# Kernel tuning notes

Hardware: AMD Instinct MI355X
Metric: run time of the kernel (lower is better)

Reference implementation:

```python
import jax, jax.numpy as jnp
import numpy as np

B, S, D, H = 2, 2048, 1024, 16

def setup_inputs() -> dict:
    key = jax.random.key(0)
    ks = jax.random.split(key, 5)
    s = 0.02
    return {
        "x": jax.random.normal(ks[0], (B, S, D), dtype=jnp.float32),
        "Wq": jax.random.normal(ks[1], (D, D), dtype=jnp.float32) * s,
        "bq": jnp.zeros((D,), dtype=jnp.float32),
        "Wk": jax.random.normal(ks[2], (D, D), dtype=jnp.float32) * s,
        "bk": jnp.zeros((D,), dtype=jnp.float32),
        "Wv": jax.random.normal(ks[3], (D, D), dtype=jnp.float32) * s,
        "bv": jnp.zeros((D,), dtype=jnp.float32),
        "Wp": jax.random.normal(ks[4], (D, D), dtype=jnp.float32) * s,
        "bp": jnp.zeros((D,), dtype=jnp.float32),
    }

def reference(x, Wq, bq, Wk, bk, Wv, bv, Wp, bp):
    b, s, d = x.shape
    hd = d // H
    # QKV projections, split into heads: [b, H, s, hd]
    q = (x @ Wq.T + bq).reshape(b, s, H, hd).transpose(0, 2, 1, 3)
    k = (x @ Wk.T + bk).reshape(b, s, H, hd).transpose(0, 2, 1, 3)
    v = (x @ Wv.T + bv).reshape(b, s, H, hd).transpose(0, 2, 1, 3)
    # NOTE: original scales by 1/sqrt(embedding_size), not head_dim
    att = jnp.einsum("bhqd,bhkd->bhqk", q, k) / jnp.sqrt(jnp.float32(d))
    causal = jnp.tril(jnp.ones((s, s), dtype=bool))
    att = jnp.where(causal[None, None], att, -jnp.inf)
    att = jax.nn.softmax(att, axis=-1)
    y = jnp.einsum("bhqk,bhkd->bhqd", att, v)
    y = y.transpose(0, 2, 1, 3).reshape(b, s, d)
    return y @ Wp.T + bp
```

## Files before the change

kernel.cpp:

```cpp
#include <hip/hip_runtime.h>
#include <hip/hip_bf16.h>

#define B_  2
#define S_  2048
#define D_  1024
#define H_  16
#define HD_ 64

typedef float  f32x4 __attribute__((ext_vector_type(4)));
typedef __bf16 bf16x8 __attribute__((ext_vector_type(8)));

__device__ __forceinline__ unsigned short f2bf(float f) {
    __bf16 h = (__bf16)f;
    return __builtin_bit_cast(unsigned short, h);
}

__device__ __forceinline__ void gload_lds16(const unsigned short* g, unsigned short* l) {
    __builtin_amdgcn_global_load_lds(
        (const __attribute__((address_space(1))) unsigned int*)g,
        (__attribute__((address_space(3))) unsigned int*)l, 16, 0, 0);
}

__global__ __launch_bounds__(256) void cvt5(
    const float* __restrict__ x,  const float* __restrict__ wq,
    const float* __restrict__ wk, const float* __restrict__ wv,
    const float* __restrict__ wp,
    unsigned short* __restrict__ xb, unsigned short* __restrict__ wqkv,
    unsigned short* __restrict__ wpb)
{
    const int bid = blockIdx.x;
    const float* src; unsigned short* dst; int off;
    if (bid < 4096)      { src = x;  dst = xb;              off = bid * 1024; }
    else if (bid < 5120) { src = wq; dst = wqkv;            off = (bid - 4096) * 1024; }
    else if (bid < 6144) { src = wk; dst = wqkv + (1<<20);  off = (bid - 5120) * 1024; }
    else if (bid < 7168) { src = wv; dst = wqkv + (2<<20);  off = (bid - 6144) * 1024; }
    else                 { src = wp; dst = wpb;             off = (bid - 7168) * 1024; }
    const int i = off + threadIdx.x * 4;
    float4 v = *reinterpret_cast<const float4*>(src + i);
    ushort4 o;
    o.x = f2bf(v.x); o.y = f2bf(v.y); o.z = f2bf(v.z); o.w = f2bf(v.w);
    *reinterpret_cast<ushort4*>(dst + i) = o;
}

template <int MODE>
__global__ __launch_bounds__(256, 2) void gemm128(
    const unsigned short* __restrict__ A,
    const unsigned short* __restrict__ Bm,
    const float* __restrict__ bias,
    void* __restrict__ C0, void* __restrict__ C1, void* __restrict__ C2,
    int M, int N, int K)
{
    __shared__ unsigned short As[128 * 64];
    __shared__ unsigned short Bs[128 * 64];
    const int tid  = threadIdx.x;
    const int lane = tid & 63;
    const int w    = tid >> 6;
    const int wm   = w >> 1, wn = w & 1;
    const int m0   = blockIdx.x << 7, n0 = blockIdx.y << 7;
    const int l15  = lane & 15, l4 = lane >> 4;
    const int r8   = lane >> 3;
    const int c8   = (lane & 7) << 3;

    f32x4 acc[4][4] = {};

    for (int k0 = 0; k0 < K; k0 += 64) {
        if (k0) __syncthreads();
        #pragma unroll
        for (int i = 0; i < 4; ++i) {
            const int row = i * 32 + w * 8;
            gload_lds16(A  + (size_t)(m0 + row + r8) * K + k0 + c8, As + row * 64);
            gload_lds16(Bm + (size_t)(n0 + row + r8) * K + k0 + c8, Bs + row * 64);
        }
        __syncthreads();
        #pragma unroll
        for (int kk = 0; kk < 2; ++kk) {
            bf16x8 af[4], bf[4];
            #pragma unroll
            for (int mi = 0; mi < 4; ++mi)
                af[mi] = *reinterpret_cast<const bf16x8*>(&As[(wm * 64 + mi * 16 + l15) * 64 + kk * 32 + l4 * 8]);
            #pragma unroll
            for (int ni = 0; ni < 4; ++ni)
                bf[ni] = *reinterpret_cast<const bf16x8*>(&Bs[(wn * 64 + ni * 16 + l15) * 64 + kk * 32 + l4 * 8]);
            #pragma unroll
            for (int mi = 0; mi < 4; ++mi)
                #pragma unroll
                for (int ni = 0; ni < 4; ++ni)
                    acc[mi][ni] = __builtin_amdgcn_mfma_f32_16x16x32_bf16(af[mi], bf[ni], acc[mi][ni], 0, 0, 0);
        }
    }

    #pragma unroll
    for (int mi = 0; mi < 4; ++mi) {
        #pragma unroll
        for (int ni = 0; ni < 4; ++ni) {
            const int colg = n0 + wn * 64 + ni * 16 + l15;
            const float bv = bias[colg];
            const int rowb = m0 + wm * 64 + mi * 16 + l4 * 4;
            if constexpr (MODE == 0) {
                float* C = (float*)C0;
                #pragma unroll
                for (int j = 0; j < 4; ++j)
                    C[(size_t)(rowb + j) * N + colg] = acc[mi][ni][j] + bv;
            } else {
                const int region = n0 >> 10;
                const int cl = colg & 1023;
                if (region < 2) {
                    unsigned short* C = (unsigned short*)(region ? C1 : C0);
                    #pragma unroll
                    for (int j = 0; j < 4; ++j)
                        C[(size_t)(rowb + j) * 1024 + cl] = f2bf(acc[mi][ni][j] + bv);
                } else {
                    ushort4 pk;
                    pk.x = f2bf(acc[mi][ni][0] + bv);
                    pk.y = f2bf(acc[mi][ni][1] + bv);
                    pk.z = f2bf(acc[mi][ni][2] + bv);
                    pk.w = f2bf(acc[mi][ni][3] + bv);
                    const int bb = rowb >> 11, s = rowb & (S_ - 1);
                    unsigned short* vt = (unsigned short*)C2 +
                        ((size_t)(bb * H_ + (cl >> 6)) * HD_ + (cl & 63)) * S_ + s;
                    *reinterpret_cast<ushort4*>(vt) = pk;
                }
            }
        }
    }
}

__global__ __launch_bounds__(256) void attn4(
    const unsigned short* __restrict__ qb,
    const unsigned short* __restrict__ kb,
    const unsigned short* __restrict__ vt,
    unsigned short* __restrict__ yb)
{
    __shared__ unsigned short Plds[4][32][80];

    const int tid  = threadIdx.x;
    const int lane = tid & 63, w = tid >> 6;
    const int l15  = lane & 15, l4 = lane >> 4;

    const int bid  = blockIdx.x;
    const int xcd  = bid & 7;
    const int seq  = bid >> 3;
    const int hb   = xcd * 4 + (seq >> 4);
    const int qt   = 15 - (seq & 15);
    const int h    = hb & 15, b = hb >> 4;

    const int q0w  = qt * 128 + w * 32;
    const size_t baseTok = (size_t)b * S_;
    const unsigned short* kgh = kb + baseTok * D_ + h * HD_;
    const unsigned short* vth = vt + (size_t)(b * H_ + h) * HD_ * S_;

    bf16x8 qf[2][2];
    #pragma unroll
    for (int m = 0; m < 2; ++m)
        #pragma unroll
        for (int kh = 0; kh < 2; ++kh)
            qf[m][kh] = *reinterpret_cast<const bf16x8*>(
                qb + (baseTok + q0w + m * 16 + l15) * D_ + h * HD_ + kh * 32 + l4 * 8);

    f32x4 o_acc[2][4] = {};
    float l_part[2][4] = {};

    const int nkv = (q0w + 95) >> 6;

    bf16x8 kf[4][2];
    #pragma unroll
    for (int kvb = 0; kvb < 4; ++kvb)
        #pragma unroll
        for (int kh = 0; kh < 2; ++kh)
            kf[kvb][kh] = *reinterpret_cast<const bf16x8*>(
                kgh + (size_t)(kvb * 16 + l15) * D_ + kh * 32 + l4 * 8);

    for (int t = 0; t < nkv; ++t) {
        const int kv0 = t << 6;

        f32x4 s[2][4] = {};
        #pragma unroll
        for (int m = 0; m < 2; ++m)
            #pragma unroll
            for (int kvb = 0; kvb < 4; ++kvb)
                #pragma unroll
                for (int kh = 0; kh < 2; ++kh)
                    s[m][kvb] = __builtin_amdgcn_mfma_f32_16x16x32_bf16(
                        qf[m][kh], kf[kvb][kh], s[m][kvb], 0, 0, 0);

        bf16x8 kn[4][2];
        if (t + 1 < nkv) {
            #pragma unroll
            for (int kvb = 0; kvb < 4; ++kvb)
                #pragma unroll
                for (int kh = 0; kh < 2; ++kh)
                    kn[kvb][kh] = *reinterpret_cast<const bf16x8*>(
                        kgh + (size_t)(kv0 + 64 + kvb * 16 + l15) * D_ + kh * 32 + l4 * 8);
        }

        bf16x8 vf[2][4];
        #pragma unroll
        for (int kvh = 0; kvh < 2; ++kvh)
            #pragma unroll
            for (int nb = 0; nb < 4; ++nb)
                vf[kvh][nb] = *reinterpret_cast<const bf16x8*>(
                    vth + (size_t)(nb * 16 + l15) * S_ + kv0 + kvh * 32 + l4 * 8);

        const bool need_mask = (kv0 + 63 > q0w);
        #pragma unroll
        for (int m = 0; m < 2; ++m) {
            #pragma unroll
            for (int j = 0; j < 4; ++j) {
                const int rowg = q0w + m * 16 + l4 * 4 + j;
                float ps = 0.f;
                #pragma unroll
                for (int kvb = 0; kvb < 4; ++kvb) {
                    const bool masked = need_mask && (kv0 + kvb * 16 + l15 > rowg);
                    const float p = masked ? 0.f : __expf(s[m][kvb][j] * 0.03125f);
                    ps += p;
                    Plds[w][m * 16 + l4 * 4 + j][kvb * 16 + l15] = f2bf(p);
                }
                l_part[m][j] += ps;
            }
        }

        #pragma unroll
        for (int kvh = 0; kvh < 2; ++kvh) {
            #pragma unroll
            for (int m = 0; m < 2; ++m) {
                bf16x8 pf = *reinterpret_cast<const bf16x8*>(&Plds[w][m * 16 + l15][kvh * 32 + l4 * 8]);
                #pragma unroll
                for (int nb = 0; nb < 4; ++nb)
                    o_acc[m][nb] = __builtin_amdgcn_mfma_f32_16x16x32_bf16(
                        pf, vf[kvh][nb], o_acc[m][nb], 0, 0, 0);
            }
        }

        #pragma unroll
        for (int kvb = 0; kvb < 4; ++kvb)
            #pragma unroll
            for (int kh = 0; kh < 2; ++kh)
                kf[kvb][kh] = kn[kvb][kh];
    }

    float l[8];
    #pragma unroll
    for (int m = 0; m < 2; ++m)
        #pragma unroll
        for (int j = 0; j < 4; ++j)
            l[m * 4 + j] = l_part[m][j];
    #pragma unroll
    for (int st = 1; st <= 8; st <<= 1) {
        float tv[8];
        #pragma unroll
        for (int i = 0; i < 8; ++i) tv[i] = __shfl_xor(l[i], st);
        #pragma unroll
        for (int i = 0; i < 8; ++i) l[i] += tv[i];
    }
    #pragma unroll
    for (int m = 0; m < 2; ++m) {
        #pragma unroll
        for (int j = 0; j < 4; ++j) {
            const float inv = 1.0f / l[m * 4 + j];
            const int rowg = q0w + m * 16 + l4 * 4 + j;
            unsigned short* yp = yb + (baseTok + rowg) * D_ + h * HD_ + l15;
            #pragma unroll
            for (int nb = 0; nb < 4; ++nb)
                yp[nb * 16] = f2bf(o_acc[m][nb][j] * inv);
        }
    }
}

extern "C" void kernel_launch(void* const* d_in, const int* in_sizes, int n_in,
                              void* d_out, int out_size, void* d_ws, size_t ws_size,
                              hipStream_t stream)
{
    const float* x  = (const float*)d_in[0];
    const float* Wq = (const float*)d_in[1];
    const float* bq = (const float*)d_in[2];
    const float* Wk = (const float*)d_in[3];
    const float* bk = (const float*)d_in[4];
    const float* Wv = (const float*)d_in[5];
    const float* bv = (const float*)d_in[6];
    const float* Wp = (const float*)d_in[7];
    const float* bp = (const float*)d_in[8];

    char* ws = (char*)d_ws;
    const size_t MB = 1024 * 1024;
    unsigned short* xb    = (unsigned short*)(ws);
    unsigned short* wqkvb = (unsigned short*)(ws + 8 * MB);
    unsigned short* wpb   = (unsigned short*)(ws + 14 * MB);
    unsigned short* qbuf  = (unsigned short*)(ws + 16 * MB);
    unsigned short* kbuf  = (unsigned short*)(ws + 24 * MB);
    unsigned short* vtbf  = (unsigned short*)(ws + 32 * MB);
    unsigned short* ybuf  = (unsigned short*)(ws + 40 * MB);
    float*          bcat  = (float*)(ws + 48 * MB);

    const int M = B_ * S_;

    cvt5<<<8192, 256, 0, stream>>>(x, Wq, Wk, Wv, Wp, xb, wqkvb, wpb);
    hipMemcpyAsync(bcat,          bq, D_ * sizeof(float), hipMemcpyDeviceToDevice, stream);
    hipMemcpyAsync(bcat + D_,     bk, D_ * sizeof(float), hipMemcpyDeviceToDevice, stream);
    hipMemcpyAsync(bcat + 2 * D_, bv, D_ * sizeof(float), hipMemcpyDeviceToDevice, stream);

    gemm128<1><<<dim3(M / 128, 3072 / 128, 1), 256, 0, stream>>>(
        xb, wqkvb, bcat, qbuf, kbuf, vtbf, M, 3072, D_);

    attn4<<<512, 256, 0, stream>>>(qbuf, kbuf, vtbf, ybuf);

    gemm128<0><<<dim3(M / 128, D_ / 128, 1), 256, 0, stream>>>(
        ybuf, wpb, bp, (float*)d_out, nullptr, nullptr, M, D_, D_);
}
```

Measured before the change: 268.9 us.

## Split attention into single-wave blocks and prioritize MFMA phases

The attention kernel now launches 2048 single-wavefront blocks, each handling 32 query rows, in place of 512 blocks of four waves. Query tiles are still issued longest-first. This is meant to let the scheduler balance the uneven causal workloads per wave and to stop short waves from holding a whole block's resources. It also wraps the MFMA sections in s_setprio and replaces __expf with exp2f using a prescaled constant. The trade-off is many more blocks, and waves of the same head no longer share a CU as they did within one block, which can hurt cache locality.

```diff
diff --git a/kernel.cpp b/kernel.cpp
--- a/kernel.cpp
+++ b/kernel.cpp
@@ -125,26 +125,25 @@
     }
 }
 
-__global__ __launch_bounds__(256) void attn4(
+__global__ __launch_bounds__(64) void attn5(
     const unsigned short* __restrict__ qb,
     const unsigned short* __restrict__ kb,
     const unsigned short* __restrict__ vt,
     unsigned short* __restrict__ yb)
 {
-    __shared__ unsigned short Plds[4][32][80];
-
-    const int tid  = threadIdx.x;
-    const int lane = tid & 63, w = tid >> 6;
+    __shared__ unsigned short Plds[32][80];
+
+    const int lane = threadIdx.x;
     const int l15  = lane & 15, l4 = lane >> 4;
 
     const int bid  = blockIdx.x;
     const int xcd  = bid & 7;
-    const int seq  = bid >> 3;
-    const int hb   = xcd * 4 + (seq >> 4);
-    const int qt   = 15 - (seq & 15);
+    const int idx  = bid >> 3;
+    const int hb   = xcd * 4 + (idx >> 6);
+    const int qi   = 63 - (idx & 63);
     const int h    = hb & 15, b = hb >> 4;
 
-    const int q0w  = qt * 128 + w * 32;
+    const int q0w  = qi * 32;
     const size_t baseTok = (size_t)b * S_;
     const unsigned short* kgh = kb + baseTok * D_ + h * HD_;
     const unsigned short* vth = vt + (size_t)(b * H_ + h) * HD_ * S_;
@@ -174,6 +173,7 @@
         const int kv0 = t << 6;
 
         f32x4 s[2][4] = {};
+        __builtin_amdgcn_s_setprio(1);
         #pragma unroll
         for (int m = 0; m < 2; ++m)
             #pragma unroll
@@ -182,6 +182,7 @@
                 for (int kh = 0; kh < 2; ++kh)
                     s[m][kvb] = __builtin_amdgcn_mfma_f32_16x16x32_bf16(
                         qf[m][kh], kf[kvb][kh], s[m][kvb], 0, 0, 0);
+        __builtin_amdgcn_s_setprio(0);
 
         bf16x8 kn[4][2];
         if (t + 1 < nkv) {
@@ -210,32 +211,36 @@
                 float ps = 0.f;
                 #pragma unroll
                 for (int kvb = 0; kvb < 4; ++kvb) {
-                    const bool masked = need_mask && (kv0 + kvb * 16 + l15 > rowg);
-                    const float p = masked ? 0.f : __expf(s[m][kvb][j] * 0.03125f);
+                    const bool ok = !need_mask || (kv0 + kvb * 16 + l15 <= rowg);
+                    const float p = ok ? exp2f(s[m][kvb][j] * 0.04508422f) : 0.f;
                     ps += p;
-                    Plds[w][m * 16 + l4 * 4 + j][kvb * 16 + l15] = f2bf(p);
+                    Plds[m * 16 + l4 * 4 + j][kvb * 16 + l15] = f2bf(p);
                 }
                 l_part[m][j] += ps;
             }
         }
 
+        __builtin_amdgcn_s_setprio(1);
         #pragma unroll
         for (int kvh = 0; kvh < 2; ++kvh) {
             #pragma unroll
             for (int m = 0; m < 2; ++m) {
-                bf16x8 pf = *reinterpret_cast<const bf16x8*>(&Plds[w][m * 16 + l15][kvh * 32 + l4 * 8]);
+                bf16x8 pf = *reinterpret_cast<const bf16x8*>(&Plds[m * 16 + l15][kvh * 32 + l4 * 8]);
                 #pragma unroll
                 for (int nb = 0; nb < 4; ++nb)
                     o_acc[m][nb] = __builtin_amdgcn_mfma_f32_16x16x32_bf16(
                         pf, vf[kvh][nb], o_acc[m][nb], 0, 0, 0);
             }
         }
-
-        #pragma unroll
-        for (int kvb = 0; kvb < 4; ++kvb)
-            #pragma unroll
-            for (int kh = 0; kh < 2; ++kh)
-                kf[kvb][kh] = kn[kvb][kh];
+        __builtin_amdgcn_s_setprio(0);
+
+        if (t + 1 < nkv) {
+            #pragma unroll
+            for (int kvb = 0; kvb < 4; ++kvb)
+                #pragma unroll
+                for (int kh = 0; kh < 2; ++kh)
+                    kf[kvb][kh] = kn[kvb][kh];
+        }
     }
 
     float l[8];
@@ -301,7 +306,7 @@
     gemm128<1><<<dim3(M / 128, 3072 / 128, 1), 256, 0, stream>>>(
         xb, wqkvb, bcat, qbuf, kbuf, vtbf, M, 3072, D_);
 
-    attn4<<<512, 256, 0, stream>>>(qbuf, kbuf, vtbf, ybuf);
+    attn5<<<2048, 64, 0, stream>>>(qbuf, kbuf, vtbf, ybuf);
 
     gemm128<0><<<dim3(M / 128, D_ / 128, 1), 256, 0, stream>>>(
         ybuf, wpb, bp, (float*)d_out, nullptr, nullptr, M, D_, D_);
```

Measured after the change: 259.7 us. 1.04x faster.
